# Optimization experiments

Hardware: AMD Instinct MI355X
Metric: run time of the kernel (lower is better)

The kernel has to match this reference:

```python
import jax, jax.numpy as jnp
import numpy as np

B, N, C = 8, 1024, 768
H, D = 12, 64
SCALE = D ** -0.5
EPS = 1e-5

def layernorm(x, g, b):
    mu = jnp.mean(x, axis=-1, keepdims=True)
    var = jnp.var(x, axis=-1, keepdims=True)
    return (x - mu) * jax.lax.rsqrt(var + EPS) * g + b

def setup_inputs() -> dict:
    key = jax.random.key(0)
    ks = jax.random.split(key, 5)
    return {
        "x": jax.random.normal(ks[0], (B, N, C), jnp.float32),
        "qkv_w": jax.random.normal(ks[1], (3 * C, C), jnp.float32) * 0.02,
        "qkv_b": jax.random.normal(ks[2], (3 * C,), jnp.float32) * 0.02,
        "qn_g": jnp.ones((D,), jnp.float32),
        "qn_b": jnp.zeros((D,), jnp.float32),
        "kn_g": jnp.ones((D,), jnp.float32),
        "kn_b": jnp.zeros((D,), jnp.float32),
        "proj_w": jax.random.normal(ks[3], (C, C), jnp.float32) * 0.02,
        "proj_b": jnp.zeros((C,), jnp.float32),
    }

def reference(x, qkv_w, qkv_b, qn_g, qn_b, kn_g, kn_b, proj_w, proj_b):
    # qkv projection: [B,N,3C] -> [3,B,H,N,D]
    qkv = jnp.einsum('bnc,oc->bno', x, qkv_w) + qkv_b
    qkv = qkv.reshape(B, N, 3, H, D).transpose(2, 0, 3, 1, 4)
    q, k, v = qkv[0], qkv[1], qkv[2]
    q = layernorm(q, qn_g, qn_b) * SCALE
    k = layernorm(k, kn_g, kn_b)
    # explicit attention matrix [B,H,N,N] (module stores it)
    attn = jax.nn.softmax(jnp.einsum('bhqd,bhkd->bhqk', q, k), axis=-1)
    out = jnp.einsum('bhqk,bhkd->bhqd', attn, v)
    out = out.transpose(0, 2, 1, 3).reshape(B, N, C)
    out = jnp.einsum('bnc,oc->bno', out, proj_w) + proj_b
    return out
```

## Files before the change

kernel.cpp:

```cpp
#include <hip/hip_runtime.h>
#include <cstdint>

#define Bz 8
#define Nn 1024
#define Cc 768
#define Hh 12
#define Dd 64
#define C3 2304
#define BN 8192

constexpr float EPS = 1e-5f;
constexpr float QSCALE = 0.125f * 1.44269504088896340736f;

typedef __attribute__((ext_vector_type(8))) short bf16x8;
typedef _Float16 f16x8 __attribute__((ext_vector_type(8)));
typedef __attribute__((ext_vector_type(4))) float f32x4;
typedef __attribute__((ext_vector_type(16))) float f32x16;

__device__ __forceinline__ short f2b(float f) {
    union { float f; unsigned u; } x; x.f = f;
    unsigned r = x.u + 0x7FFFu + ((x.u >> 16) & 1u);
    return (short)(r >> 16);
}
__device__ __forceinline__ unsigned cvtpk(float a, float b) {
    unsigned r;
    asm("v_cvt_pk_bf16_f32 %0, %1, %2" : "=v"(r) : "v"(a), "v"(b));
    return r;
}

__device__ __forceinline__ f32x4 MFMAH(f16x8 a, f16x8 b, f32x4 c) {
    return __builtin_amdgcn_mfma_f32_16x16x32_f16(a, b, c, 0, 0, 0);
}
__device__ __forceinline__ f32x16 MFMA32(bf16x8 a, bf16x8 b, f32x16 c) {
    return __builtin_amdgcn_mfma_f32_32x32x16_bf16(a, b, c, 0, 0, 0);
}
__device__ __forceinline__ f16x8 ldf16(const _Float16* p) { return *(const f16x8*)p; }
__device__ __forceinline__ void gld16(const void* g, void* l) {
    __builtin_amdgcn_global_load_lds((const __attribute__((address_space(1))) unsigned int*)g,
                                     (__attribute__((address_space(3))) unsigned int*)(l),
                                     16, 0, 0);
}

__global__ __launch_bounds__(256) void cvt_all(
    const float* __restrict__ x, const float* __restrict__ wq, const float* __restrict__ wp,
    _Float16* __restrict__ xh, _Float16* __restrict__ wqh, _Float16* __restrict__ wph)
{
    const int n1 = BN * Cc / 8, n2 = n1 + C3 * Cc / 8, n3 = n2 + Cc * Cc / 8;
    int i = blockIdx.x * 256 + threadIdx.x;
    const float* s; _Float16* d; int off;
    if (i < n1)      { s = x;  d = xh;  off = i; }
    else if (i < n2) { s = wq; d = wqh; off = i - n1; }
    else if (i < n3) { s = wp; d = wph; off = i - n2; }
    else return;
    float4 a = *(const float4*)(s + (size_t)off * 8);
    float4 b = *(const float4*)(s + (size_t)off * 8 + 4);
    f16x8 o;
    o[0] = (_Float16)a.x; o[1] = (_Float16)a.y; o[2] = (_Float16)a.z; o[3] = (_Float16)a.w;
    o[4] = (_Float16)b.x; o[5] = (_Float16)b.y; o[6] = (_Float16)b.z; o[7] = (_Float16)b.w;
    *(f16x8*)(d + (size_t)off * 8) = o;
}

template<int EPI>
__global__ __launch_bounds__(256) void gemm_f16(
    const _Float16* __restrict__ A,
    const _Float16* __restrict__ W,
    const float* __restrict__ bias,
    float* __restrict__ Out,
    short* __restrict__ qp, short* __restrict__ kp, short* __restrict__ vp,
    const float* __restrict__ qg, const float* __restrict__ qb,
    const float* __restrict__ kg, const float* __restrict__ kb)
{
    __shared__ _Float16 As[128 * 64];
    __shared__ _Float16 Bs[128 * 64];
    const int tid = threadIdx.x;
    const int lane = tid & 63;
    const int w = tid >> 6;
    const int wr = w >> 1, wc = w & 1;
    const int l15 = lane & 15, l4 = lane >> 4;
    const int m0 = blockIdx.y * 128;
    const int n0 = blockIdx.x * 128;
    const int lr = lane >> 3;
    const int lslot = lane & 7;

    f32x4 acc[4][4];
#pragma unroll
    for (int mi = 0; mi < 4; ++mi)
#pragma unroll
        for (int ni = 0; ni < 4; ++ni) { acc[mi][ni][0]=0.f; acc[mi][ni][1]=0.f; acc[mi][ni][2]=0.f; acc[mi][ni][3]=0.f; }

    for (int kt = 0; kt < 12; ++kt) {
        const int k0 = kt * 64;
#pragma unroll
        for (int j = 0; j < 8; ++j) {
            int i = w * 8 + j;
            int isA = (i < 16);
            int ib = isA ? i : i - 16;
            int row = ib * 8 + lr;
            int gslot = lslot ^ (row & 7);
            const _Float16* src = (isA ? A + (size_t)(m0 + row) * 768
                                       : W + (size_t)(n0 + row) * 768) + k0 + gslot * 8;
            _Float16* dst = (isA ? As : Bs) + ib * 512;
            gld16(src, dst);
        }
        __syncthreads();
#pragma unroll
        for (int ks = 0; ks < 2; ++ks) {
            f16x8 af[4], bfr[4];
#pragma unroll
            for (int mi = 0; mi < 4; ++mi) {
                int row = wr * 64 + mi * 16 + l15;
                int slot = (ks * 4 + l4) ^ (row & 7);
                af[mi] = ldf16(&As[row * 64 + slot * 8]);
            }
#pragma unroll
            for (int ni = 0; ni < 4; ++ni) {
                int row = wc * 64 + ni * 16 + l15;
                int slot = (ks * 4 + l4) ^ (row & 7);
                bfr[ni] = ldf16(&Bs[row * 64 + slot * 8]);
            }
#pragma unroll
            for (int mi = 0; mi < 4; ++mi)
#pragma unroll
                for (int ni = 0; ni < 4; ++ni)
                    acc[mi][ni] = MFMAH(af[mi], bfr[ni], acc[mi][ni]);
        }
        __syncthreads();
    }

    if (EPI == 0) {
#pragma unroll
        for (int mi = 0; mi < 4; ++mi)
#pragma unroll
            for (int r = 0; r < 4; ++r) {
                int row = m0 + wr * 64 + mi * 16 + l4 * 4 + r;
#pragma unroll
                for (int ni = 0; ni < 4; ++ni) {
                    int col = n0 + wc * 64 + ni * 16 + l15;
                    Out[(size_t)row * Cc + col] = acc[mi][ni][r] + bias[col];
                }
            }
    } else {
        const int ncol0 = n0 + wc * 64;
        const int type = ncol0 / Cc;
        const int h = (ncol0 % Cc) >> 6;
        const float* gptr = (type == 0) ? qg : kg;
        const float* bptr = (type == 0) ? qb : kb;
        float biasv[4], gv[4], bv[4];
#pragma unroll
        for (int ni = 0; ni < 4; ++ni) {
            int d = ni * 16 + l15;
            biasv[ni] = bias[ncol0 + d];
            if (type < 2) { gv[ni] = gptr[d]; bv[ni] = bptr[d]; }
        }
        short* plane = (type == 0) ? qp : (type == 1) ? kp : vp;
#pragma unroll
        for (int mi = 0; mi < 4; ++mi)
#pragma unroll
            for (int r = 0; r < 4; ++r) {
                float v[4];
#pragma unroll
                for (int ni = 0; ni < 4; ++ni) v[ni] = acc[mi][ni][r] + biasv[ni];
                int row = m0 + wr * 64 + mi * 16 + l4 * 4 + r;
                size_t base = ((size_t)row * Hh + h) * 64;
                if (type < 2) {
                    float s = v[0] + v[1] + v[2] + v[3];
#pragma unroll
                    for (int off = 1; off < 16; off <<= 1) s += __shfl_xor(s, off);
                    float mu = s * (1.0f / 64.0f);
                    float s2 = 0.f;
#pragma unroll
                    for (int ni = 0; ni < 4; ++ni) { float dv = v[ni] - mu; s2 += dv * dv; }
#pragma unroll
                    for (int off = 1; off < 16; off <<= 1) s2 += __shfl_xor(s2, off);
                    float inv = rsqrtf(s2 * (1.0f / 64.0f) + EPS);
#pragma unroll
                    for (int ni = 0; ni < 4; ++ni) {
                        float rr = (v[ni] - mu) * inv * gv[ni] + bv[ni];
                        if (type == 0) rr *= QSCALE;
                        plane[base + ni * 16 + l15] = f2b(rr);
                    }
                } else {
#pragma unroll
                    for (int ni = 0; ni < 4; ++ni)
                        plane[base + ni * 16 + l15] = f2b(v[ni]);
                }
            }
    }
}

__global__ __launch_bounds__(256, 4) void flash_attn_mfma(
    const short* __restrict__ qp, const short* __restrict__ kp, const short* __restrict__ vp,
    _Float16* __restrict__ att)
{
    __shared__ short kls[2][64 * 64];
    __shared__ short vtl[2][64 * 64];
    const int tid = threadIdx.x;
    const int lane = tid & 63;
    const int w = tid >> 6;
    const int l31 = lane & 31;
    const int hi = lane >> 5;
    const int lr = lane >> 3;
    const int lslot = lane & 7;
    const int bid = (blockIdx.x & 7) * 96 + (blockIdx.x >> 3);
    const int qt = bid & 7;
    const int bh = bid >> 3;
    const int h = bh % Hh;
    const int b = bh / Hh;
    const int q0 = qt * 128;
    const size_t hbase = ((size_t)b * Nn * Hh + h) * 64;
    const int n0v = (tid & 31) * 2, d0v = (tid >> 5) * 8;

    bf16x8 qf[4];
    {
        const short* qsrc = qp + hbase + (size_t)(q0 + w * 32 + l31) * 768 + hi * 8;
#pragma unroll
        for (int ds = 0; ds < 4; ++ds)
            qf[ds] = *(const bf16x8*)(qsrc + ds * 16);
    }

#pragma unroll
    for (int i = 0; i < 2; ++i) {
        int rl = i * 32 + w * 8 + lr;
        gld16(kp + hbase + (size_t)rl * 768 + (lslot ^ lr) * 8,
              &kls[0][(i * 32 + w * 8) * 64]);
    }
    {
        const short* s0 = vp + hbase + (size_t)n0v * 768 + d0v;
        bf16x8 a0 = *(const bf16x8*)s0;
        bf16x8 a1 = *(const bf16x8*)(s0 + 768);
#pragma unroll
        for (int j = 0; j < 8; ++j) {
            int d = d0v + j;
            unsigned pk = (unsigned short)a0[j] | ((unsigned)(unsigned short)a1[j] << 16);
            *(unsigned*)&vtl[0][d * 64 + (((n0v >> 3) ^ (d & 7)) << 3) + (n0v & 7)] = pk;
        }
    }
    __syncthreads();

    f32x16 o0, o1;
#pragma unroll
    for (int i = 0; i < 16; ++i) { o0[i] = 0.f; o1[i] = 0.f; }
    float lrun = 0.f;
    unsigned afu[4][4];

    for (int kt = 0; kt < 16; ++kt) {
        const int cur = kt & 1, nxt = cur ^ 1;
        bf16x8 va0, va1;
        if (kt < 15) {
#pragma unroll
            for (int i = 0; i < 2; ++i) {
                int rl = i * 32 + w * 8 + lr;
                gld16(kp + hbase + (size_t)((kt + 1) * 64 + rl) * 768 + (lslot ^ lr) * 8,
                      &kls[nxt][(i * 32 + w * 8) * 64]);
            }
            const short* s0 = vp + hbase + (size_t)((kt + 1) * 64 + n0v) * 768 + d0v;
            va0 = *(const bf16x8*)s0;
            va1 = *(const bf16x8*)(s0 + 768);
        }
#pragma unroll
        for (int t2 = 0; t2 < 2; ++t2) {
            f32x16 st;
#pragma unroll
            for (int i = 0; i < 16; ++i) st[i] = 0.f;
            const int row = t2 * 32 + l31;
            const int rsw = row & 7;
#pragma unroll
            for (int ds = 0; ds < 4; ++ds) {
                bf16x8 kf = *(const bf16x8*)&kls[cur][row * 64 + (((ds * 2 + hi) ^ rsw) << 3)];
                st = MFMA32(kf, qf[ds], st);
            }
#pragma unroll
            for (int i = 0; i < 16; ++i) { st[i] = exp2f(st[i]); lrun += st[i]; }
            unsigned pk[8], sx[8];
#pragma unroll
            for (int i = 0; i < 8; ++i) pk[i] = cvtpk(st[2 * i], st[2 * i + 1]);
#pragma unroll
            for (int i = 0; i < 8; ++i) sx[i] = (unsigned)__shfl_xor((int)pk[i], 32);
            afu[t2 * 2 + 0][0] = hi ? sx[2] : pk[0];
            afu[t2 * 2 + 0][1] = hi ? sx[3] : pk[1];
            afu[t2 * 2 + 0][2] = hi ? pk[2] : sx[0];
            afu[t2 * 2 + 0][3] = hi ? pk[3] : sx[1];
            afu[t2 * 2 + 1][0] = hi ? sx[6] : pk[4];
            afu[t2 * 2 + 1][1] = hi ? sx[7] : pk[5];
            afu[t2 * 2 + 1][2] = hi ? pk[6] : sx[4];
            afu[t2 * 2 + 1][3] = hi ? pk[7] : sx[5];
        }
        __builtin_amdgcn_s_setprio(1);
#pragma unroll
        for (int c = 0; c < 4; ++c) {
            union { bf16x8 v; unsigned u[4]; } a;
            a.u[0] = afu[c][0]; a.u[1] = afu[c][1]; a.u[2] = afu[c][2]; a.u[3] = afu[c][3];
            const int r0 = l31, r1 = 32 + l31;
            const int sw = l31 & 7;
            bf16x8 vf0 = *(const bf16x8*)&vtl[cur][r0 * 64 + (((c * 2 + hi) ^ sw) << 3)];
            bf16x8 vf1 = *(const bf16x8*)&vtl[cur][r1 * 64 + (((c * 2 + hi) ^ sw) << 3)];
            o0 = MFMA32(a.v, vf0, o0);
            o1 = MFMA32(a.v, vf1, o1);
        }
        __builtin_amdgcn_s_setprio(0);
        if (kt < 15) {
#pragma unroll
            for (int j = 0; j < 8; ++j) {
                int d = d0v + j;
                unsigned pk = (unsigned short)va0[j] | ((unsigned)(unsigned short)va1[j] << 16);
                *(unsigned*)&vtl[nxt][d * 64 + (((n0v >> 3) ^ (d & 7)) << 3) + (n0v & 7)] = pk;
            }
        }
        __syncthreads();
    }

    lrun += __shfl_xor(lrun, 32);
    float linv = 1.0f / lrun;
#pragma unroll
    for (int r = 0; r < 16; ++r) {
        int qr = (r & 3) + 8 * (r >> 2) + 4 * hi;
        float invr = __shfl(linv, qr);
        int row = q0 + w * 32 + qr;
        _Float16* dst = att + (size_t)(b * Nn + row) * Cc + h * 64 + l31;
        dst[0]  = (_Float16)(o0[r] * invr);
        dst[32] = (_Float16)(o1[r] * invr);
    }
}

extern "C" void kernel_launch(void* const* d_in, const int* in_sizes, int n_in,
                              void* d_out, int out_size, void* d_ws, size_t ws_size,
                              hipStream_t stream)
{
    const float* x      = (const float*)d_in[0];
    const float* qkv_w  = (const float*)d_in[1];
    const float* qkv_b  = (const float*)d_in[2];
    const float* qn_g   = (const float*)d_in[3];
    const float* qn_b   = (const float*)d_in[4];
    const float* kn_g   = (const float*)d_in[5];
    const float* kn_b   = (const float*)d_in[6];
    const float* proj_w = (const float*)d_in[7];
    const float* proj_b = (const float*)d_in[8];
    float* out = (float*)d_out;

    char* ws = (char*)d_ws;
    short*    qp  = (short*)(ws);
    short*    kp  = (short*)(ws + 12582912);
    short*    vp  = (short*)(ws + 25165824);
    _Float16* att = (_Float16*)(ws + 37748736);
    _Float16* xh  = (_Float16*)(ws + 50331648);
    _Float16* wqh = (_Float16*)(ws + 62914560);
    _Float16* wph = (_Float16*)(ws + 66453504);

    {
        const int n3 = BN * Cc / 8 + C3 * Cc / 8 + Cc * Cc / 8;
        cvt_all<<<(n3 + 255) / 256, 256, 0, stream>>>(x, qkv_w, proj_w, xh, wqh, wph);
    }
    gemm_f16<1><<<dim3(C3 / 128, BN / 128), 256, 0, stream>>>(
        xh, wqh, qkv_b, nullptr, qp, kp, vp, qn_g, qn_b, kn_g, kn_b);
    flash_attn_mfma<<<Bz * Hh * 8, 256, 0, stream>>>(qp, kp, vp, att);
    gemm_f16<0><<<dim3(Cc / 128, BN / 128), 256, 0, stream>>>(
        att, wph, proj_b, out, nullptr, nullptr, nullptr, nullptr, nullptr, nullptr, nullptr);
}
```

Measured before the change: 133.0 us.

## Double-buffer GEMM LDS tiles and remap blocks for XCD locality

The f16 GEMM now keeps two LDS buffers, so the global-to-LDS load of the next K tile is issued before the MFMA work on the current tile, overlapping memory latency with compute. The 2D grid becomes a 1D grid whose block index is spread across the 8 XCDs in contiguous chunks and walks tile rows in serpentine order, to improve L2 reuse of A rows and W tiles. A launch-bounds hint asks for two blocks per CU. The cost is double the LDS footprint (64 KB per block) and register pressure from the occupancy hint, which could cause spills.

```diff
diff --git a/kernel.cpp b/kernel.cpp
--- a/kernel.cpp
+++ b/kernel.cpp
@@ -61,34 +61,37 @@
 }
 
 template<int EPI>
-__global__ __launch_bounds__(256) void gemm_f16(
+__global__ __launch_bounds__(256, 2) void gemm_f16(
     const _Float16* __restrict__ A,
     const _Float16* __restrict__ W,
     const float* __restrict__ bias,
     float* __restrict__ Out,
     short* __restrict__ qp, short* __restrict__ kp, short* __restrict__ vp,
     const float* __restrict__ qg, const float* __restrict__ qb,
-    const float* __restrict__ kg, const float* __restrict__ kb)
+    const float* __restrict__ kg, const float* __restrict__ kb,
+    int nx)
 {
-    __shared__ _Float16 As[128 * 64];
-    __shared__ _Float16 Bs[128 * 64];
+    __shared__ _Float16 As[2][128 * 64];
+    __shared__ _Float16 Bs[2][128 * 64];
     const int tid = threadIdx.x;
     const int lane = tid & 63;
     const int w = tid >> 6;
     const int wr = w >> 1, wc = w & 1;
     const int l15 = lane & 15, l4 = lane >> 4;
-    const int m0 = blockIdx.y * 128;
-    const int n0 = blockIdx.x * 128;
     const int lr = lane >> 3;
     const int lslot = lane & 7;
 
-    f32x4 acc[4][4];
-#pragma unroll
-    for (int mi = 0; mi < 4; ++mi)
-#pragma unroll
-        for (int ni = 0; ni < 4; ++ni) { acc[mi][ni][0]=0.f; acc[mi][ni][1]=0.f; acc[mi][ni][2]=0.f; acc[mi][ni][3]=0.f; }
-
-    for (int kt = 0; kt < 12; ++kt) {
+    {
+    }
+    const int chunk = gridDim.x >> 3;
+    const int wg = (blockIdx.x & 7) * chunk + (blockIdx.x >> 3);
+    const int by = wg / nx;
+    int bx = wg % nx;
+    if (by & 1) bx = nx - 1 - bx;
+    const int m0 = by * 128;
+    const int n0 = bx * 128;
+
+    auto stage = [&](int kt, int buf) {
         const int k0 = kt * 64;
 #pragma unroll
         for (int j = 0; j < 8; ++j) {
@@ -99,10 +102,23 @@
             int gslot = lslot ^ (row & 7);
             const _Float16* src = (isA ? A + (size_t)(m0 + row) * 768
                                        : W + (size_t)(n0 + row) * 768) + k0 + gslot * 8;
-            _Float16* dst = (isA ? As : Bs) + ib * 512;
+            _Float16* dst = (isA ? &As[buf][0] : &Bs[buf][0]) + ib * 512;
             gld16(src, dst);
         }
-        __syncthreads();
+    };
+
+    f32x4 acc[4][4];
+#pragma unroll
+    for (int mi = 0; mi < 4; ++mi)
+#pragma unroll
+        for (int ni = 0; ni < 4; ++ni) { acc[mi][ni][0]=0.f; acc[mi][ni][1]=0.f; acc[mi][ni][2]=0.f; acc[mi][ni][3]=0.f; }
+
+    stage(0, 0);
+    __syncthreads();
+
+    for (int kt = 0; kt < 12; ++kt) {
+        const int cur = kt & 1;
+        if (kt < 11) stage(kt + 1, cur ^ 1);
 #pragma unroll
         for (int ks = 0; ks < 2; ++ks) {
             f16x8 af[4], bfr[4];
@@ -110,13 +126,13 @@
             for (int mi = 0; mi < 4; ++mi) {
                 int row = wr * 64 + mi * 16 + l15;
                 int slot = (ks * 4 + l4) ^ (row & 7);
-                af[mi] = ldf16(&As[row * 64 + slot * 8]);
+                af[mi] = ldf16(&As[cur][row * 64 + slot * 8]);
             }
 #pragma unroll
             for (int ni = 0; ni < 4; ++ni) {
                 int row = wc * 64 + ni * 16 + l15;
                 int slot = (ks * 4 + l4) ^ (row & 7);
-                bfr[ni] = ldf16(&Bs[row * 64 + slot * 8]);
+                bfr[ni] = ldf16(&Bs[cur][row * 64 + slot * 8]);
             }
 #pragma unroll
             for (int mi = 0; mi < 4; ++mi)
@@ -350,9 +366,9 @@
         const int n3 = BN * Cc / 8 + C3 * Cc / 8 + Cc * Cc / 8;
         cvt_all<<<(n3 + 255) / 256, 256, 0, stream>>>(x, qkv_w, proj_w, xh, wqh, wph);
     }
-    gemm_f16<1><<<dim3(C3 / 128, BN / 128), 256, 0, stream>>>(
-        xh, wqh, qkv_b, nullptr, qp, kp, vp, qn_g, qn_b, kn_g, kn_b);
+    gemm_f16<1><<<(BN / 128) * (C3 / 128), 256, 0, stream>>>(
+        xh, wqh, qkv_b, nullptr, qp, kp, vp, qn_g, qn_b, kn_g, kn_b, C3 / 128);
     flash_attn_mfma<<<Bz * Hh * 8, 256, 0, stream>>>(qp, kp, vp, att);
-    gemm_f16<0><<<dim3(Cc / 128, BN / 128), 256, 0, stream>>>(
-        att, wph, proj_b, out, nullptr, nullptr, nullptr, nullptr, nullptr, nullptr, nullptr);
-}
+    gemm_f16<0><<<(BN / 128) * (Cc / 128), 256, 0, stream>>>(
+        att, wph, proj_b, out, nullptr, nullptr, nullptr, nullptr, nullptr, nullptr, nullptr, Cc / 128);
+}
```

After: 128.0 us. 3.7% less time.
